# Optimization experiments

Hardware: AMD Instinct MI355X
Metric: run time of the kernel (lower is better)

The kernel has to match this reference:

```python
import jax, jax.numpy as jnp
import numpy as np

N_NODES = 100000
N_EDGES = 1600000
D_IN = 128
D_HID = 128
D_OUT = 128


def sage_conv(x, src, dst, W_l, b_l, W_r, n_nodes):
    # PyG SAGEConv (mean aggr): out = Linear_l(mean_j x_j) + Linear_r(x_i)
    msg = x[src]                                            # [E, d] gather
    agg = jax.ops.segment_sum(msg, dst, num_segments=n_nodes)  # [N, d]
    cnt = jax.ops.segment_sum(jnp.ones((src.shape[0],), x.dtype), dst,
                              num_segments=n_nodes)
    mean = agg / jnp.maximum(cnt, 1.0)[:, None]             # mean over neighbors
    return mean @ W_l.T + b_l + x @ W_r.T


def setup_inputs() -> dict:
    key = jax.random.key(0)
    ks = jax.random.split(key, 8)
    x = jax.random.normal(ks[0], (N_NODES, D_IN), dtype=jnp.float32)
    edge_index = jax.random.randint(ks[1], (2, N_EDGES), 0, N_NODES, dtype=jnp.int64)
    s1 = 1.0 / np.sqrt(D_IN)
    s2 = 1.0 / np.sqrt(D_HID)
    W1_l = jax.random.uniform(ks[2], (D_HID, D_IN), jnp.float32, -s1, s1)
    b1_l = jax.random.uniform(ks[3], (D_HID,), jnp.float32, -s1, s1)
    W1_r = jax.random.uniform(ks[4], (D_HID, D_IN), jnp.float32, -s1, s1)
    W2_l = jax.random.uniform(ks[5], (D_OUT, D_HID), jnp.float32, -s2, s2)
    b2_l = jax.random.uniform(ks[6], (D_OUT,), jnp.float32, -s2, s2)
    W2_r = jax.random.uniform(ks[7], (D_OUT, D_HID), jnp.float32, -s2, s2)
    return {"x": x, "edge_index": edge_index, "W1_l": W1_l, "b1_l": b1_l,
            "W1_r": W1_r, "W2_l": W2_l, "b2_l": b2_l, "W2_r": W2_r}


def reference(x, edge_index, W1_l, b1_l, W1_r, W2_l, b2_l, W2_r):
    src, dst = edge_index[0], edge_index[1]
    n = x.shape[0]
    h = sage_conv(x, src, dst, W1_l, b1_l, W1_r, n)
    h = jax.nn.relu(h)
    # F.dropout with training=False (eval mode) is identity
    out = sage_conv(h, src, dst, W2_l, b2_l, W2_r, n)
    return out
```

## Files before the change

### kernel.cpp

```cpp
#include <hip/hip_runtime.h>

typedef __attribute__((ext_vector_type(8))) short short8;
typedef __attribute__((ext_vector_type(4))) float f32x4;
typedef __attribute__((ext_vector_type(2))) float f32x2;

#define NBMAX 512
#define CAP 8192

__device__ inline unsigned short f2bf(float f) {
  union { float f; unsigned u; } v; v.f = f;
  unsigned r = v.u + 0x7fffu + ((v.u >> 16) & 1u);
  return (unsigned short)(r >> 16);
}

__device__ inline void addf2(f32x2 (&a)[4], uint4 v) {
  union { uint2 u; f32x2 f; } t;
  t.u.x = v.x << 16; t.u.y = v.x & 0xffff0000u; a[0] += t.f;
  t.u.x = v.y << 16; t.u.y = v.y & 0xffff0000u; a[1] += t.f;
  t.u.x = v.z << 16; t.u.y = v.z & 0xffff0000u; a[2] += t.f;
  t.u.x = v.w << 16; t.u.y = v.w & 0xffff0000u; a[3] += t.f;
}

__device__ inline int load_src(const int* ei, int E, int e, int f64) {
  return f64 ? ei[2 * e] : ei[e];
}
__device__ inline int load_dst(const int* ei, int E, int e, int f64) {
  return f64 ? ei[2 * (E + e)] : ei[E + e];
}

__global__ __launch_bounds__(256) void prep(
    const int* __restrict__ ei, int E,
    int* __restrict__ btot, int2* __restrict__ stage, int SB,
    const float* __restrict__ x, unsigned short* __restrict__ xb, int n8,
    const float* __restrict__ W1l, const float* __restrict__ W1r,
    const float* __restrict__ W2l, const float* __restrict__ W2r,
    unsigned short* __restrict__ Wp) {
  __shared__ int lcnt[NBMAX];
  __shared__ int lbase[NBMAX];
  __shared__ int sflag;
  const int b = blockIdx.x;
  const int t = threadIdx.x;

  if (b < SB) {
    if (t == 0) sflag = 0;
    for (int i = t; i < NBMAX; i += 256) lcnt[i] = 0;
    __syncthreads();
    const int e0 = b * 4096;
    {
      int e = e0 + t;
      int v = (e < E) ? ei[2 * e + 1] : 0;
      if (v) atomicOr(&sflag, 1);
    }
    __syncthreads();
    const int f64 = (sflag == 0) ? 1 : 0;

    int srcs[16], bks[16];
    int dsts[16];
#pragma unroll
    for (int i = 0; i < 16; ++i) {
      int e = e0 + i * 256 + t;
      if (e < E) {
        srcs[i] = load_src(ei, E, e, f64);
        int d = load_dst(ei, E, e, f64);
        dsts[i] = d;
        bks[i] = d >> 8;
        atomicAdd(&lcnt[d >> 8], 1);
      } else {
        bks[i] = -1;
      }
    }
    __syncthreads();
    for (int i = t; i < NBMAX; i += 256) {
      int c = lcnt[i];
      lbase[i] = c ? atomicAdd(&btot[i], c) : 0;
    }
    __syncthreads();
    for (int i = t; i < NBMAX; i += 256) lcnt[i] = 0;
    __syncthreads();
#pragma unroll
    for (int i = 0; i < 16; ++i) {
      int bk = bks[i];
      if (bk >= 0) {
        int r = atomicAdd(&lcnt[bk], 1);
        stage[(size_t)bk * CAP + lbase[bk] + r] = make_int2(srcs[i], dsts[i]);
      }
    }
    return;
  }

  if (b < SB + 4) {
    const int m = b - SB;
    const float* W = (m == 0) ? W1l : (m == 1) ? W1r : (m == 2) ? W2l : W2r;
    unsigned short* dst = Wp + (size_t)m * 16384;
#pragma unroll
    for (int it = 0; it < 8; ++it) {
      int id = it * 256 + t;
      int j = id >> 4;
      int kc = id & 15;
      int s = kc >> 2, q = kc & 3;
      int jt = j >> 4, nn2 = j & 15;
      int c = (s * 8 + jt) * 4 + q;
      const float* src = W + j * 128 + kc * 8;
      union { unsigned short u[8]; uint4 v; } tv;
#pragma unroll
      for (int k = 0; k < 8; ++k) tv.u[k] = f2bf(src[k]);
      *(uint4*)(dst + (c * 16 + nn2) * 8) = tv.v;
    }
    return;
  }

  const int cb = b - SB - 4;
  const int nxb = gridDim.x - SB - 4;
  int i = cb * 256 + t;
  const int stride = nxb * 256;
  for (; i < n8; i += stride) {
    float4 v0 = ((const float4*)x)[2 * i];
    float4 v1 = ((const float4*)x)[2 * i + 1];
    union { unsigned short u[8]; uint4 v; } tv;
    tv.u[0] = f2bf(v0.x); tv.u[1] = f2bf(v0.y);
    tv.u[2] = f2bf(v0.z); tv.u[3] = f2bf(v0.w);
    tv.u[4] = f2bf(v1.x); tv.u[5] = f2bf(v1.y);
    tv.u[6] = f2bf(v1.z); tv.u[7] = f2bf(v1.w);
    ((uint4*)xb)[i] = tv.v;
  }
}

__global__ __launch_bounds__(256) void bucket_fill2(
    const int2* __restrict__ stage, const int* __restrict__ btot,
    int* __restrict__ offs, int* __restrict__ cnt, float* __restrict__ inv,
    int* __restrict__ csr, int N) {
  __shared__ int lhist[256];
  __shared__ int lscan[256];
  __shared__ int lcur[256];
  __shared__ int red[256];
  const int b = blockIdx.x;
  const int t = threadIdx.x;
  int sum = 0;
  for (int j = t; j < b; j += 256) sum += btot[j];
  red[t] = sum;
  lhist[t] = 0;
  __syncthreads();
  for (int d = 128; d; d >>= 1) {
    if (t < d) red[t] += red[t + d];
    __syncthreads();
  }
  const int base = red[0];
  const int count = btot[b];
  const int2* sp = stage + (size_t)b * CAP;
  for (int i = t; i < count; i += 256)
    atomicAdd(&lhist[sp[i].y & 255], 1);
  __syncthreads();
  int v = lhist[t];
  lscan[t] = v;
  __syncthreads();
  for (int d = 1; d < 256; d <<= 1) {
    int tv = (t >= d) ? lscan[t - d] : 0;
    __syncthreads();
    lscan[t] += tv;
    __syncthreads();
  }
  const int excl = lscan[t] - v;
  const int node = b * 256 + t;
  if (node < N) {
    offs[node] = base + excl;
    cnt[node] = v;
    inv[node] = 1.0f / (float)((v > 1) ? v : 1);
  }
  lcur[t] = base + excl;
  __syncthreads();
  for (int i = t; i < count; i += 256) {
    int2 sd = sp[i];
    int p = atomicAdd(&lcur[sd.y & 255], 1);
    csr[p] = sd.x;
  }
}

__global__ __launch_bounds__(256, 4) void agg_mean(
    const unsigned short* __restrict__ A, const float* __restrict__ inv,
    const int* __restrict__ offs, const int* __restrict__ cnt,
    const int* __restrict__ csr, unsigned short* __restrict__ M, int n) {
  int pr = (int)((blockIdx.x * 256 + threadIdx.x) >> 6);
  int n0 = pr * 2;
  if (n0 >= n) return;
  const int n1 = n0 + 1;
  const bool has1 = (n1 < n);
  const int lane = threadIdx.x & 63;
  const int g = lane >> 4;
  const int l = lane & 15;
  const int deg0 = cnt[n0];
  const int deg1 = has1 ? cnt[n1] : 0;
  const int start = offs[n0];
  const int T = deg0 + deg1;
  f32x2 acc0[4] = {{0.f, 0.f}, {0.f, 0.f}, {0.f, 0.f}, {0.f, 0.f}};
  f32x2 acc1[4] = {{0.f, 0.f}, {0.f, 0.f}, {0.f, 0.f}, {0.f, 0.f}};
  const char* Ab = (const char*)A + (size_t)l * 16;

  if (T <= 64) {
    int offb = ((lane < T) ? csr[start + lane] : 0) << 8;
    {
      int nb[8];
      uint4 vv[8];
#pragma unroll
      for (int j = 0; j < 8; ++j) nb[j] = __shfl(offb, j * 4 + g);
#pragma unroll
      for (int j = 0; j < 8; ++j)
        vv[j] = *(const uint4*)(Ab + (size_t)(unsigned)nb[j]);
#pragma unroll
      for (int j = 0; j < 8; ++j) {
        int e = j * 4 + g;
        if (e < deg0) addf2(acc0, vv[j]);
        else if (e < T) addf2(acc1, vv[j]);
      }
    }
    if (T > 32) {
      int nb[8];
      uint4 vv[8];
#pragma unroll
      for (int j = 0; j < 8; ++j) nb[j] = __shfl(offb, 32 + j * 4 + g);
#pragma unroll
      for (int j = 0; j < 8; ++j)
        vv[j] = *(const uint4*)(Ab + (size_t)(unsigned)nb[j]);
#pragma unroll
      for (int j = 0; j < 8; ++j) {
        int e = 32 + j * 4 + g;
        if (e < deg0) addf2(acc0, vv[j]);
        else if (e < T) addf2(acc1, vv[j]);
      }
    }
  } else {
    for (int node = 0; node < 2; ++node) {
      int dg = node ? deg1 : deg0;
      int st = node ? (start + deg0) : start;
      for (int base = 0; base < dg; base += 64) {
        int m = dg - base;
        if (m > 64) m = 64;
        int offb = ((lane < m) ? csr[st + base + lane] : 0) << 8;
#pragma unroll 4
        for (int i = 0; i < m; i += 4) {
          int sl = i + g;
          int nbv = __shfl(offb, sl & 63);
          if (sl < m) {
            uint4 v = *(const uint4*)(Ab + (size_t)(unsigned)nbv);
            if (node) addf2(acc1, v);
            else addf2(acc0, v);
          }
        }
      }
    }
  }

#pragma unroll
  for (int k = 0; k < 4; ++k) {
    acc0[k].x += __shfl_xor(acc0[k].x, 16);
    acc0[k].x += __shfl_xor(acc0[k].x, 32);
    acc0[k].y += __shfl_xor(acc0[k].y, 16);
    acc0[k].y += __shfl_xor(acc0[k].y, 32);
    acc1[k].x += __shfl_xor(acc1[k].x, 16);
    acc1[k].x += __shfl_xor(acc1[k].x, 32);
    acc1[k].y += __shfl_xor(acc1[k].y, 16);
    acc1[k].y += __shfl_xor(acc1[k].y, 32);
  }

  const int c0 = l * 8 + g * 2;
  {
    float s = inv[n0];
    unsigned pkt = (unsigned)f2bf(acc0[g].x * s) |
                   ((unsigned)f2bf(acc0[g].y * s) << 16);
    *(unsigned*)(M + (size_t)n0 * 128 + c0) = pkt;
  }
  if (has1) {
    float s = inv[n1];
    unsigned pkt = (unsigned)f2bf(acc1[g].x * s) |
                   ((unsigned)f2bf(acc1[g].y * s) << 16);
    *(unsigned*)(M + (size_t)n1 * 128 + c0) = pkt;
  }
}

template <int RELU, int OUTBF>
__global__ __launch_bounds__(256) void gemm_fused(
    const unsigned short* __restrict__ Am,
    const unsigned short* __restrict__ As,
    const unsigned short* __restrict__ Wp,
    const float* __restrict__ bias, void* __restrict__ outp, int n) {
  __shared__ unsigned short wsh[2 * 16384];
  const int tid = threadIdx.x;

  {
    const uint4* wsrc = (const uint4*)Wp;
    uint4* wdst = (uint4*)wsh;
#pragma unroll
    for (int it = 0; it < 16; ++it) {
      int id = it * 256 + tid;
      wdst[id] = wsrc[id];
    }
  }
  __syncthreads();

  const int lane = tid & 63;
  const int wave = tid >> 6;
  const int nn = lane & 15;
  const int quad = lane >> 4;
  const int rowbase = blockIdx.x * 64 + wave * 16;

  int nodeA = rowbase + nn;
  if (nodeA > n - 1) nodeA = n - 1;

  short8 am[4], asf[4];
#pragma unroll
  for (int s = 0; s < 4; ++s) {
    am[s] = *(const short8*)(Am + (size_t)nodeA * 128 + s * 32 + quad * 8);
    asf[s] = *(const short8*)(As + (size_t)nodeA * 128 + s * 32 + quad * 8);
  }

  f32x4 acc[8];
#pragma unroll
  for (int jt = 0; jt < 8; ++jt) acc[jt] = (f32x4){0.f, 0.f, 0.f, 0.f};

#pragma unroll
  for (int jt = 0; jt < 8; ++jt) {
#pragma unroll
    for (int s = 0; s < 4; ++s) {
      int c = (s * 8 + jt) * 4 + quad;
      short8 bl = *(const short8*)(wsh + (c * 16 + nn) * 8);
      short8 br = *(const short8*)(wsh + 16384 + (c * 16 + nn) * 8);
      acc[jt] = __builtin_amdgcn_mfma_f32_16x16x32_bf16(am[s], bl, acc[jt], 0, 0, 0);
      acc[jt] = __builtin_amdgcn_mfma_f32_16x16x32_bf16(asf[s], br, acc[jt], 0, 0, 0);
    }
  }

#pragma unroll
  for (int jt = 0; jt < 8; ++jt) {
    int col = jt * 16 + nn;
    float bv = bias[col];
#pragma unroll
    for (int r = 0; r < 4; ++r) {
      int ro = rowbase + quad * 4 + r;
      if (ro < n) {
        float o = acc[jt][r] + bv;
        if (RELU) o = fmaxf(o, 0.f);
        if (OUTBF) {
          ((unsigned short*)outp)[(size_t)ro * 128 + col] = f2bf(o);
        } else {
          ((float*)outp)[(size_t)ro * 128 + col] = o;
        }
      }
    }
  }
}


extern "C" void kernel_launch(void* const* d_in, const int* in_sizes, int n_in,
                              void* d_out, int out_size, void* d_ws, size_t ws_size,
                              hipStream_t stream) {
  const float* x = (const float*)d_in[0];
  const int* ei = (const int*)d_in[1];
  const float* W1l = (const float*)d_in[2];
  const float* b1 = (const float*)d_in[3];
  const float* W1r = (const float*)d_in[4];
  const float* W2l = (const float*)d_in[5];
  const float* b2 = (const float*)d_in[6];
  const float* W2r = (const float*)d_in[7];
  float* out = (float*)d_out;

  const int N = in_sizes[0] / 128;
  const int E = in_sizes[1] / 2;
  const int nb = (N + 255) / 256;

  char* p = (char*)d_ws;
  auto alloc = [&](size_t bytes) {
    char* r = p;
    p += (bytes + 255) & ~(size_t)255;
    return r;
  };
  int* btot = (int*)alloc((size_t)NBMAX * 4);
  int* cnt = (int*)alloc((size_t)N * 4);
  int* offs = (int*)alloc((size_t)N * 4);
  float* inv = (float*)alloc((size_t)N * 4);
  int* csr = (int*)alloc((size_t)E * 4);
  unsigned short* Mb = (unsigned short*)alloc((size_t)N * 128 * 2);
  unsigned short* Wpb = (unsigned short*)alloc((size_t)4 * 16384 * 2);
  size_t stage_bytes = (size_t)nb * CAP * 8;
  size_t hb_bytes = (size_t)N * 128 * 2;
  char* shared_region = alloc(stage_bytes > hb_bytes ? stage_bytes : hb_bytes);
  unsigned short* hb = (unsigned short*)shared_region;
  int2* stage = (int2*)shared_region;

  unsigned short* xb = (unsigned short*)d_out;

  hipMemsetAsync(btot, 0, (size_t)nb * 4, stream);

  const int SB = (E + 4095) / 4096;
  prep<<<SB + 4 + 2048, 256, 0, stream>>>(ei, E, btot, stage, SB,
                                          x, xb, N * 128 / 8,
                                          W1l, W1r, W2l, W2r, Wpb);
  bucket_fill2<<<nb, 256, 0, stream>>>(stage, btot, offs, cnt, inv, csr, N);

  const int gb = (N + 63) / 64;
  const int pairs = (N + 1) / 2;
  const int ab2 = (pairs + 3) / 4;

  agg_mean<<<ab2, 256, 0, stream>>>(xb, inv, offs, cnt, csr, Mb, N);
  gemm_fused<1, 1><<<gb, 256, 0, stream>>>(Mb, xb, Wpb, b1, (void*)hb, N);
  agg_mean<<<ab2, 256, 0, stream>>>(hb, inv, offs, cnt, csr, Mb, N);
  gemm_fused<0, 0><<<gb, 256, 0, stream>>>(Mb, hb, Wpb + 32768, b2, (void*)out, N);
}
```

Measured before the change: 323.7 us.

## Fuse neighbor mean aggregation into the MFMA GEMM kernel per layer

Replaces the separate agg_mean and gemm_fused kernels with one agg_gemm kernel. Each lane gathers and averages the neighbor rows of its own node straight into registers as the bf16 A-operand, so the intermediate mean buffer is never written to or read back from global memory. The two weight halves are now staged one after the other through a single 32KB LDS buffer, which halves shared-memory use per block. The cost is a different gather pattern: each lane walks its node's edge list serially with only two edges in flight, and all 16 nodes in a group loop to the largest degree among them. This gives less coalescing and less memory-level parallelism than the old wavefront-per-node-pair gather.

```diff
diff --git a/kernel.cpp b/kernel.cpp
--- a/kernel.cpp
+++ b/kernel.cpp
@@ -175,126 +175,22 @@
   }
 }
 
-__global__ __launch_bounds__(256, 4) void agg_mean(
-    const unsigned short* __restrict__ A, const float* __restrict__ inv,
+template <int RELU, int OUTBF>
+__global__ __launch_bounds__(256, 4) void agg_gemm(
+    const unsigned short* __restrict__ A,
+    const unsigned short* __restrict__ Wp,
+    const float* __restrict__ bias, const float* __restrict__ inv,
     const int* __restrict__ offs, const int* __restrict__ cnt,
-    const int* __restrict__ csr, unsigned short* __restrict__ M, int n) {
-  int pr = (int)((blockIdx.x * 256 + threadIdx.x) >> 6);
-  int n0 = pr * 2;
-  if (n0 >= n) return;
-  const int n1 = n0 + 1;
-  const bool has1 = (n1 < n);
-  const int lane = threadIdx.x & 63;
-  const int g = lane >> 4;
-  const int l = lane & 15;
-  const int deg0 = cnt[n0];
-  const int deg1 = has1 ? cnt[n1] : 0;
-  const int start = offs[n0];
-  const int T = deg0 + deg1;
-  f32x2 acc0[4] = {{0.f, 0.f}, {0.f, 0.f}, {0.f, 0.f}, {0.f, 0.f}};
-  f32x2 acc1[4] = {{0.f, 0.f}, {0.f, 0.f}, {0.f, 0.f}, {0.f, 0.f}};
-  const char* Ab = (const char*)A + (size_t)l * 16;
-
-  if (T <= 64) {
-    int offb = ((lane < T) ? csr[start + lane] : 0) << 8;
-    {
-      int nb[8];
-      uint4 vv[8];
-#pragma unroll
-      for (int j = 0; j < 8; ++j) nb[j] = __shfl(offb, j * 4 + g);
-#pragma unroll
-      for (int j = 0; j < 8; ++j)
-        vv[j] = *(const uint4*)(Ab + (size_t)(unsigned)nb[j]);
-#pragma unroll
-      for (int j = 0; j < 8; ++j) {
-        int e = j * 4 + g;
-        if (e < deg0) addf2(acc0, vv[j]);
-        else if (e < T) addf2(acc1, vv[j]);
-      }
-    }
-    if (T > 32) {
-      int nb[8];
-      uint4 vv[8];
-#pragma unroll
-      for (int j = 0; j < 8; ++j) nb[j] = __shfl(offb, 32 + j * 4 + g);
-#pragma unroll
-      for (int j = 0; j < 8; ++j)
-        vv[j] = *(const uint4*)(Ab + (size_t)(unsigned)nb[j]);
-#pragma unroll
-      for (int j = 0; j < 8; ++j) {
-        int e = 32 + j * 4 + g;
-        if (e < deg0) addf2(acc0, vv[j]);
-        else if (e < T) addf2(acc1, vv[j]);
-      }
-    }
-  } else {
-    for (int node = 0; node < 2; ++node) {
-      int dg = node ? deg1 : deg0;
-      int st = node ? (start + deg0) : start;
-      for (int base = 0; base < dg; base += 64) {
-        int m = dg - base;
-        if (m > 64) m = 64;
-        int offb = ((lane < m) ? csr[st + base + lane] : 0) << 8;
-#pragma unroll 4
-        for (int i = 0; i < m; i += 4) {
-          int sl = i + g;
-          int nbv = __shfl(offb, sl & 63);
-          if (sl < m) {
-            uint4 v = *(const uint4*)(Ab + (size_t)(unsigned)nbv);
-            if (node) addf2(acc1, v);
-            else addf2(acc0, v);
-          }
-        }
-      }
-    }
-  }
-
-#pragma unroll
-  for (int k = 0; k < 4; ++k) {
-    acc0[k].x += __shfl_xor(acc0[k].x, 16);
-    acc0[k].x += __shfl_xor(acc0[k].x, 32);
-    acc0[k].y += __shfl_xor(acc0[k].y, 16);
-    acc0[k].y += __shfl_xor(acc0[k].y, 32);
-    acc1[k].x += __shfl_xor(acc1[k].x, 16);
-    acc1[k].x += __shfl_xor(acc1[k].x, 32);
-    acc1[k].y += __shfl_xor(acc1[k].y, 16);
-    acc1[k].y += __shfl_xor(acc1[k].y, 32);
-  }
-
-  const int c0 = l * 8 + g * 2;
-  {
-    float s = inv[n0];
-    unsigned pkt = (unsigned)f2bf(acc0[g].x * s) |
-                   ((unsigned)f2bf(acc0[g].y * s) << 16);
-    *(unsigned*)(M + (size_t)n0 * 128 + c0) = pkt;
-  }
-  if (has1) {
-    float s = inv[n1];
-    unsigned pkt = (unsigned)f2bf(acc1[g].x * s) |
-                   ((unsigned)f2bf(acc1[g].y * s) << 16);
-    *(unsigned*)(M + (size_t)n1 * 128 + c0) = pkt;
-  }
-}
-
-template <int RELU, int OUTBF>
-__global__ __launch_bounds__(256) void gemm_fused(
-    const unsigned short* __restrict__ Am,
-    const unsigned short* __restrict__ As,
-    const unsigned short* __restrict__ Wp,
-    const float* __restrict__ bias, void* __restrict__ outp, int n) {
-  __shared__ unsigned short wsh[2 * 16384];
+    const int* __restrict__ csr, void* __restrict__ outp, int n) {
+  __shared__ unsigned short wsh[16384];
   const int tid = threadIdx.x;
 
   {
     const uint4* wsrc = (const uint4*)Wp;
     uint4* wdst = (uint4*)wsh;
 #pragma unroll
-    for (int it = 0; it < 16; ++it) {
-      int id = it * 256 + tid;
-      wdst[id] = wsrc[id];
-    }
-  }
-  __syncthreads();
+    for (int it = 0; it < 8; ++it) wdst[it * 256 + tid] = wsrc[it * 256 + tid];
+  }
 
   const int lane = tid & 63;
   const int wave = tid >> 6;
@@ -305,16 +201,70 @@
   int nodeA = rowbase + nn;
   if (nodeA > n - 1) nodeA = n - 1;
 
-  short8 am[4], asf[4];
+  short8 asf[4];
+#pragma unroll
+  for (int s = 0; s < 4; ++s)
+    asf[s] = *(const short8*)(A + (size_t)nodeA * 128 + s * 32 + quad * 8);
+
+  const int deg = cnt[nodeA];
+  const int off0 = offs[nodeA];
+  const float sc = inv[nodeA];
+
+  int md = deg;
+  md = max(md, __shfl_xor(md, 1));
+  md = max(md, __shfl_xor(md, 2));
+  md = max(md, __shfl_xor(md, 4));
+  md = max(md, __shfl_xor(md, 8));
+
+  f32x2 acc[4][4];
+#pragma unroll
+  for (int s = 0; s < 4; ++s)
+#pragma unroll
+    for (int p = 0; p < 4; ++p) acc[s][p] = (f32x2){0.f, 0.f};
+
+  const char* Abase = (const char*)A;
+  const int qoff = quad * 16;
+
+  int i0 = (0 < deg) ? csr[off0] : 0;
+  int i1 = (1 < deg) ? csr[off0 + 1] : 0;
+  for (int j = 0; j < md; j += 2) {
+    int ni0 = (j + 2 < deg) ? csr[off0 + j + 2] : 0;
+    int ni1 = (j + 3 < deg) ? csr[off0 + j + 3] : 0;
+    const char* p0 = Abase + ((size_t)(unsigned)i0 << 8) + qoff;
+    const char* p1 = Abase + ((size_t)(unsigned)i1 << 8) + qoff;
+    uint4 v0[4], v1[4];
+#pragma unroll
+    for (int s = 0; s < 4; ++s) v0[s] = *(const uint4*)(p0 + s * 64);
+#pragma unroll
+    for (int s = 0; s < 4; ++s) v1[s] = *(const uint4*)(p1 + s * 64);
+    if (j < deg) {
+#pragma unroll
+      for (int s = 0; s < 4; ++s) addf2(acc[s], v0[s]);
+    }
+    if (j + 1 < deg) {
+#pragma unroll
+      for (int s = 0; s < 4; ++s) addf2(acc[s], v1[s]);
+    }
+    i0 = ni0; i1 = ni1;
+  }
+
+  short8 am[4];
 #pragma unroll
   for (int s = 0; s < 4; ++s) {
-    am[s] = *(const short8*)(Am + (size_t)nodeA * 128 + s * 32 + quad * 8);
-    asf[s] = *(const short8*)(As + (size_t)nodeA * 128 + s * 32 + quad * 8);
-  }
-
-  f32x4 acc[8];
-#pragma unroll
-  for (int jt = 0; jt < 8; ++jt) acc[jt] = (f32x4){0.f, 0.f, 0.f, 0.f};
+    union { unsigned short u[8]; short8 v; } t;
+#pragma unroll
+    for (int p = 0; p < 4; ++p) {
+      t.u[2 * p] = f2bf(acc[s][p].x * sc);
+      t.u[2 * p + 1] = f2bf(acc[s][p].y * sc);
+    }
+    am[s] = t.v;
+  }
+
+  f32x4 accc[8];
+#pragma unroll
+  for (int jt = 0; jt < 8; ++jt) accc[jt] = (f32x4){0.f, 0.f, 0.f, 0.f};
+
+  __syncthreads();
 
 #pragma unroll
   for (int jt = 0; jt < 8; ++jt) {
@@ -322,9 +272,27 @@
     for (int s = 0; s < 4; ++s) {
       int c = (s * 8 + jt) * 4 + quad;
       short8 bl = *(const short8*)(wsh + (c * 16 + nn) * 8);
-      short8 br = *(const short8*)(wsh + 16384 + (c * 16 + nn) * 8);
-      acc[jt] = __builtin_amdgcn_mfma_f32_16x16x32_bf16(am[s], bl, acc[jt], 0, 0, 0);
-      acc[jt] = __builtin_amdgcn_mfma_f32_16x16x32_bf16(asf[s], br, acc[jt], 0, 0, 0);
+      accc[jt] = __builtin_amdgcn_mfma_f32_16x16x32_bf16(am[s], bl, accc[jt], 0, 0, 0);
+    }
+  }
+
+  __syncthreads();
+
+  {
+    const uint4* wsrc = (const uint4*)(Wp + 16384);
+    uint4* wdst = (uint4*)wsh;
+#pragma unroll
+    for (int it = 0; it < 8; ++it) wdst[it * 256 + tid] = wsrc[it * 256 + tid];
+  }
+  __syncthreads();
+
+#pragma unroll
+  for (int jt = 0; jt < 8; ++jt) {
+#pragma unroll
+    for (int s = 0; s < 4; ++s) {
+      int c = (s * 8 + jt) * 4 + quad;
+      short8 br = *(const short8*)(wsh + (c * 16 + nn) * 8);
+      accc[jt] = __builtin_amdgcn_mfma_f32_16x16x32_bf16(asf[s], br, accc[jt], 0, 0, 0);
     }
   }
 
@@ -336,7 +304,7 @@
     for (int r = 0; r < 4; ++r) {
       int ro = rowbase + quad * 4 + r;
       if (ro < n) {
-        float o = acc[jt][r] + bv;
+        float o = accc[jt][r] + bv;
         if (RELU) o = fmaxf(o, 0.f);
         if (OUTBF) {
           ((unsigned short*)outp)[(size_t)ro * 128 + col] = f2bf(o);
@@ -377,7 +345,6 @@
   int* offs = (int*)alloc((size_t)N * 4);
   float* inv = (float*)alloc((size_t)N * 4);
   int* csr = (int*)alloc((size_t)E * 4);
-  unsigned short* Mb = (unsigned short*)alloc((size_t)N * 128 * 2);
   unsigned short* Wpb = (unsigned short*)alloc((size_t)4 * 16384 * 2);
   size_t stage_bytes = (size_t)nb * CAP * 8;
   size_t hb_bytes = (size_t)N * 128 * 2;
@@ -396,11 +363,9 @@
   bucket_fill2<<<nb, 256, 0, stream>>>(stage, btot, offs, cnt, inv, csr, N);
 
   const int gb = (N + 63) / 64;
-  const int pairs = (N + 1) / 2;
-  const int ab2 = (pairs + 3) / 4;
-
-  agg_mean<<<ab2, 256, 0, stream>>>(xb, inv, offs, cnt, csr, Mb, N);
-  gemm_fused<1, 1><<<gb, 256, 0, stream>>>(Mb, xb, Wpb, b1, (void*)hb, N);
-  agg_mean<<<ab2, 256, 0, stream>>>(hb, inv, offs, cnt, csr, Mb, N);
-  gemm_fused<0, 0><<<gb, 256, 0, stream>>>(Mb, hb, Wpb + 32768, b2, (void*)out, N);
-}
+
+  agg_gemm<1, 1><<<gb, 256, 0, stream>>>(xb, Wpb, b1, inv, offs, cnt, csr,
+                                         (void*)hb, N);
+  agg_gemm<0, 0><<<gb, 256, 0, stream>>>(hb, Wpb + 32768, b2, inv, offs, cnt, csr,
+                                         (void*)out, N);
+}
```

Measured after the change: 329.4 us. About the same (+1.8%).

## Fuse all stages into one cooperative persistent kernel with grid syncs

Applied to the files above, without the earlier changes.

Replaces the six separate launches (prep, bucket fill, two aggregations, two GEMMs) with a single cooperative kernel of 512-thread blocks that loops over work units and separates stages with grid-wide barriers. The aim is to remove kernel launch gaps and per-kernel ramp-up and tail costs. In exchange, each block reserves 64KB of shared memory and the grid is capped to resident blocks, which can lower occupancy for the latency-bound gather phases, and every grid barrier drains the whole device.

```diff
diff --git a/kernel.cpp b/kernel.cpp
--- a/kernel.cpp
+++ b/kernel.cpp
@@ -1,4 +1,7 @@
 #include <hip/hip_runtime.h>
+#include <hip/hip_cooperative_groups.h>
+
+namespace cg = cooperative_groups;
 
 typedef __attribute__((ext_vector_type(8))) short short8;
 typedef __attribute__((ext_vector_type(4))) float f32x4;
@@ -28,92 +31,252 @@
   return f64 ? ei[2 * (E + e)] : ei[E + e];
 }
 
-__global__ __launch_bounds__(256) void prep(
-    const int* __restrict__ ei, int E,
-    int* __restrict__ btot, int2* __restrict__ stage, int SB,
-    const float* __restrict__ x, unsigned short* __restrict__ xb, int n8,
-    const float* __restrict__ W1l, const float* __restrict__ W1r,
-    const float* __restrict__ W2l, const float* __restrict__ W2r,
-    unsigned short* __restrict__ Wp) {
-  __shared__ int lcnt[NBMAX];
-  __shared__ int lbase[NBMAX];
-  __shared__ int sflag;
-  const int b = blockIdx.x;
+__device__ void agg_phase(const unsigned short* __restrict__ A,
+                          const float* __restrict__ inv,
+                          const int* __restrict__ offs,
+                          const int* __restrict__ cnt,
+                          const int* __restrict__ csr,
+                          unsigned short* __restrict__ M, int n) {
   const int t = threadIdx.x;
-
-  if (b < SB) {
-    if (t == 0) sflag = 0;
-    for (int i = t; i < NBMAX; i += 256) lcnt[i] = 0;
-    __syncthreads();
-    const int e0 = b * 4096;
+  const int lane = t & 63;
+  const int wave = t >> 6;
+  const int g = lane >> 4;
+  const int l = lane & 15;
+  const char* Ab = (const char*)A + (size_t)l * 16;
+  const int units = (((n + 1) >> 1) + 7) >> 3;
+
+  for (int u = blockIdx.x; u < units; u += gridDim.x) {
+    const int pr = u * 8 + wave;
+    const int n0 = pr * 2;
+    if (n0 >= n) continue;
+    const int n1 = n0 + 1;
+    const bool has1 = (n1 < n);
+    const int deg0 = cnt[n0];
+    const int deg1 = has1 ? cnt[n1] : 0;
+    const int start = offs[n0];
+    const int T = deg0 + deg1;
+    f32x2 acc0[4] = {{0.f, 0.f}, {0.f, 0.f}, {0.f, 0.f}, {0.f, 0.f}};
+    f32x2 acc1[4] = {{0.f, 0.f}, {0.f, 0.f}, {0.f, 0.f}, {0.f, 0.f}};
+
+    if (T <= 64) {
+      int offb = ((lane < T) ? csr[start + lane] : 0) << 8;
+      {
+        int nb2[8];
+        uint4 vv[8];
+#pragma unroll
+        for (int j = 0; j < 8; ++j) nb2[j] = __shfl(offb, j * 4 + g);
+#pragma unroll
+        for (int j = 0; j < 8; ++j)
+          vv[j] = *(const uint4*)(Ab + (size_t)(unsigned)nb2[j]);
+#pragma unroll
+        for (int j = 0; j < 8; ++j) {
+          int e = j * 4 + g;
+          if (e < deg0) addf2(acc0, vv[j]);
+          else if (e < T) addf2(acc1, vv[j]);
+        }
+      }
+      if (T > 32) {
+        int nb2[8];
+        uint4 vv[8];
+#pragma unroll
+        for (int j = 0; j < 8; ++j) nb2[j] = __shfl(offb, 32 + j * 4 + g);
+#pragma unroll
+        for (int j = 0; j < 8; ++j)
+          vv[j] = *(const uint4*)(Ab + (size_t)(unsigned)nb2[j]);
+#pragma unroll
+        for (int j = 0; j < 8; ++j) {
+          int e = 32 + j * 4 + g;
+          if (e < deg0) addf2(acc0, vv[j]);
+          else if (e < T) addf2(acc1, vv[j]);
+        }
+      }
+    } else {
+      for (int node = 0; node < 2; ++node) {
+        int dg = node ? deg1 : deg0;
+        int st = node ? (start + deg0) : start;
+        for (int base = 0; base < dg; base += 64) {
+          int m = dg - base;
+          if (m > 64) m = 64;
+          int offb = ((lane < m) ? csr[st + base + lane] : 0) << 8;
+#pragma unroll 4
+          for (int i = 0; i < m; i += 4) {
+            int sl = i + g;
+            int nbv = __shfl(offb, sl & 63);
+            if (sl < m) {
+              uint4 v = *(const uint4*)(Ab + (size_t)(unsigned)nbv);
+              if (node) addf2(acc1, v);
+              else addf2(acc0, v);
+            }
+          }
+        }
+      }
+    }
+
+#pragma unroll
+    for (int k = 0; k < 4; ++k) {
+      acc0[k].x += __shfl_xor(acc0[k].x, 16);
+      acc0[k].x += __shfl_xor(acc0[k].x, 32);
+      acc0[k].y += __shfl_xor(acc0[k].y, 16);
+      acc0[k].y += __shfl_xor(acc0[k].y, 32);
+      acc1[k].x += __shfl_xor(acc1[k].x, 16);
+      acc1[k].x += __shfl_xor(acc1[k].x, 32);
+      acc1[k].y += __shfl_xor(acc1[k].y, 16);
+      acc1[k].y += __shfl_xor(acc1[k].y, 32);
+    }
+
+    const int c0 = l * 8 + g * 2;
     {
-      int e = e0 + t;
-      int v = (e < E) ? ei[2 * e + 1] : 0;
-      if (v) atomicOr(&sflag, 1);
-    }
-    __syncthreads();
-    const int f64 = (sflag == 0) ? 1 : 0;
-
-    int srcs[16], bks[16];
-    int dsts[16];
-#pragma unroll
-    for (int i = 0; i < 16; ++i) {
-      int e = e0 + i * 256 + t;
-      if (e < E) {
-        srcs[i] = load_src(ei, E, e, f64);
-        int d = load_dst(ei, E, e, f64);
-        dsts[i] = d;
-        bks[i] = d >> 8;
-        atomicAdd(&lcnt[d >> 8], 1);
-      } else {
-        bks[i] = -1;
-      }
-    }
-    __syncthreads();
-    for (int i = t; i < NBMAX; i += 256) {
-      int c = lcnt[i];
-      lbase[i] = c ? atomicAdd(&btot[i], c) : 0;
-    }
-    __syncthreads();
-    for (int i = t; i < NBMAX; i += 256) lcnt[i] = 0;
-    __syncthreads();
-#pragma unroll
-    for (int i = 0; i < 16; ++i) {
-      int bk = bks[i];
-      if (bk >= 0) {
-        int r = atomicAdd(&lcnt[bk], 1);
-        stage[(size_t)bk * CAP + lbase[bk] + r] = make_int2(srcs[i], dsts[i]);
-      }
-    }
-    return;
-  }
-
-  if (b < SB + 4) {
-    const int m = b - SB;
-    const float* W = (m == 0) ? W1l : (m == 1) ? W1r : (m == 2) ? W2l : W2r;
-    unsigned short* dst = Wp + (size_t)m * 16384;
-#pragma unroll
-    for (int it = 0; it < 8; ++it) {
-      int id = it * 256 + t;
-      int j = id >> 4;
-      int kc = id & 15;
-      int s = kc >> 2, q = kc & 3;
-      int jt = j >> 4, nn2 = j & 15;
-      int c = (s * 8 + jt) * 4 + q;
-      const float* src = W + j * 128 + kc * 8;
-      union { unsigned short u[8]; uint4 v; } tv;
-#pragma unroll
-      for (int k = 0; k < 8; ++k) tv.u[k] = f2bf(src[k]);
-      *(uint4*)(dst + (c * 16 + nn2) * 8) = tv.v;
-    }
-    return;
-  }
-
-  const int cb = b - SB - 4;
-  const int nxb = gridDim.x - SB - 4;
-  int i = cb * 256 + t;
-  const int stride = nxb * 256;
-  for (; i < n8; i += stride) {
+      float s = inv[n0];
+      unsigned pkt = (unsigned)f2bf(acc0[g].x * s) |
+                     ((unsigned)f2bf(acc0[g].y * s) << 16);
+      *(unsigned*)(M + (size_t)n0 * 128 + c0) = pkt;
+    }
+    if (has1) {
+      float s = inv[n1];
+      unsigned pkt = (unsigned)f2bf(acc1[g].x * s) |
+                     ((unsigned)f2bf(acc1[g].y * s) << 16);
+      *(unsigned*)(M + (size_t)n1 * 128 + c0) = pkt;
+    }
+  }
+}
+
+template <int RELU, int OUTBF>
+__device__ void gemm_phase(const unsigned short* __restrict__ Am,
+                           const unsigned short* __restrict__ As,
+                           const unsigned short* __restrict__ Wp,
+                           const float* __restrict__ bias,
+                           void* __restrict__ outp, int n,
+                           unsigned short* wsh) {
+  const int tid = threadIdx.x;
+  {
+    const uint4* wsrc = (const uint4*)Wp;
+    uint4* wdst = (uint4*)wsh;
+#pragma unroll
+    for (int it = 0; it < 8; ++it)
+      wdst[it * 512 + tid] = wsrc[it * 512 + tid];
+  }
+  __syncthreads();
+
+  const int lane = tid & 63;
+  const int wave = tid >> 6;
+  const int nn = lane & 15;
+  const int quad = lane >> 4;
+  const int nch = (n + 127) >> 7;
+
+  for (int ch = blockIdx.x; ch < nch; ch += gridDim.x) {
+    const int rowbase = ch * 128 + wave * 16;
+    int nodeA = rowbase + nn;
+    if (nodeA > n - 1) nodeA = n - 1;
+
+    short8 am[4], asf[4];
+#pragma unroll
+    for (int s = 0; s < 4; ++s) {
+      am[s] = *(const short8*)(Am + (size_t)nodeA * 128 + s * 32 + quad * 8);
+      asf[s] = *(const short8*)(As + (size_t)nodeA * 128 + s * 32 + quad * 8);
+    }
+
+    f32x4 acc[8];
+#pragma unroll
+    for (int jt = 0; jt < 8; ++jt) acc[jt] = (f32x4){0.f, 0.f, 0.f, 0.f};
+
+#pragma unroll
+    for (int jt = 0; jt < 8; ++jt) {
+#pragma unroll
+      for (int s = 0; s < 4; ++s) {
+        int c = (s * 8 + jt) * 4 + quad;
+        short8 bl = *(const short8*)(wsh + (c * 16 + nn) * 8);
+        short8 br = *(const short8*)(wsh + 16384 + (c * 16 + nn) * 8);
+        acc[jt] = __builtin_amdgcn_mfma_f32_16x16x32_bf16(am[s], bl, acc[jt], 0, 0, 0);
+        acc[jt] = __builtin_amdgcn_mfma_f32_16x16x32_bf16(asf[s], br, acc[jt], 0, 0, 0);
+      }
+    }
+
+#pragma unroll
+    for (int jt = 0; jt < 8; ++jt) {
+      int col = jt * 16 + nn;
+      float bv = bias[col];
+#pragma unroll
+      for (int r = 0; r < 4; ++r) {
+        int ro = rowbase + quad * 4 + r;
+        if (ro < n) {
+          float o = acc[jt][r] + bv;
+          if (RELU) o = fmaxf(o, 0.f);
+          if (OUTBF) {
+            ((unsigned short*)outp)[(size_t)ro * 128 + col] = f2bf(o);
+          } else {
+            ((float*)outp)[(size_t)ro * 128 + col] = o;
+          }
+        }
+      }
+    }
+  }
+}
+
+__global__ __launch_bounds__(512, 4) void mega(
+    const int* __restrict__ ei, int E, int SB, int N, int nb, int n8,
+    const float* __restrict__ x,
+    const float* __restrict__ W1l, const float* __restrict__ b1,
+    const float* __restrict__ W1r, const float* __restrict__ W2l,
+    const float* __restrict__ b2, const float* __restrict__ W2r,
+    int* btot, int2* stage, int* cnt, int* offs, float* inv, int* csr,
+    unsigned short* Mb, unsigned short* Wp, unsigned short* xb,
+    unsigned short* hb, float* out) {
+  __shared__ __align__(16) int sbuf[16384];
+  cg::grid_group gg = cg::this_grid();
+  const int t = threadIdx.x;
+
+  {
+    int* lcnt = sbuf;
+    int* lbase = sbuf + NBMAX;
+    int* sflag = sbuf + 2 * NBMAX;
+    for (int c = blockIdx.x; c < SB; c += gridDim.x) {
+      if (t == 0) *sflag = 0;
+      for (int i = t; i < NBMAX; i += 512) lcnt[i] = 0;
+      __syncthreads();
+      const int e0 = c * 4096;
+      {
+        int e = e0 + t;
+        int v = (e < E) ? ei[2 * e + 1] : 0;
+        if (v) atomicOr(sflag, 1);
+      }
+      __syncthreads();
+      const int f64 = (*sflag == 0) ? 1 : 0;
+
+      int srcs[8], bks[8], dsts[8];
+#pragma unroll
+      for (int i = 0; i < 8; ++i) {
+        int e = e0 + i * 512 + t;
+        if (e < E) {
+          srcs[i] = load_src(ei, E, e, f64);
+          int d = load_dst(ei, E, e, f64);
+          dsts[i] = d;
+          bks[i] = d >> 8;
+          atomicAdd(&lcnt[d >> 8], 1);
+        } else {
+          bks[i] = -1;
+        }
+      }
+      __syncthreads();
+      for (int i = t; i < NBMAX; i += 512) {
+        int cc = lcnt[i];
+        lbase[i] = cc ? atomicAdd(&btot[i], cc) : 0;
+      }
+      __syncthreads();
+      for (int i = t; i < NBMAX; i += 512) lcnt[i] = 0;
+      __syncthreads();
+#pragma unroll
+      for (int i = 0; i < 8; ++i) {
+        int bk = bks[i];
+        if (bk >= 0) {
+          int r = atomicAdd(&lcnt[bk], 1);
+          stage[(size_t)bk * CAP + lbase[bk] + r] = make_int2(srcs[i], dsts[i]);
+        }
+      }
+      __syncthreads();
+    }
+  }
+
+  for (int i = blockIdx.x * 512 + t; i < n8; i += gridDim.x * 512) {
     float4 v0 = ((const float4*)x)[2 * i];
     float4 v1 = ((const float4*)x)[2 * i + 1];
     union { unsigned short u[8]; uint4 v; } tv;
@@ -123,229 +286,96 @@
     tv.u[6] = f2bf(v1.z); tv.u[7] = f2bf(v1.w);
     ((uint4*)xb)[i] = tv.v;
   }
-}
-
-__global__ __launch_bounds__(256) void bucket_fill2(
-    const int2* __restrict__ stage, const int* __restrict__ btot,
-    int* __restrict__ offs, int* __restrict__ cnt, float* __restrict__ inv,
-    int* __restrict__ csr, int N) {
-  __shared__ int lhist[256];
-  __shared__ int lscan[256];
-  __shared__ int lcur[256];
-  __shared__ int red[256];
-  const int b = blockIdx.x;
-  const int t = threadIdx.x;
-  int sum = 0;
-  for (int j = t; j < b; j += 256) sum += btot[j];
-  red[t] = sum;
-  lhist[t] = 0;
-  __syncthreads();
-  for (int d = 128; d; d >>= 1) {
-    if (t < d) red[t] += red[t + d];
-    __syncthreads();
-  }
-  const int base = red[0];
-  const int count = btot[b];
-  const int2* sp = stage + (size_t)b * CAP;
-  for (int i = t; i < count; i += 256)
-    atomicAdd(&lhist[sp[i].y & 255], 1);
-  __syncthreads();
-  int v = lhist[t];
-  lscan[t] = v;
-  __syncthreads();
-  for (int d = 1; d < 256; d <<= 1) {
-    int tv = (t >= d) ? lscan[t - d] : 0;
-    __syncthreads();
-    lscan[t] += tv;
-    __syncthreads();
-  }
-  const int excl = lscan[t] - v;
-  const int node = b * 256 + t;
-  if (node < N) {
-    offs[node] = base + excl;
-    cnt[node] = v;
-    inv[node] = 1.0f / (float)((v > 1) ? v : 1);
-  }
-  lcur[t] = base + excl;
-  __syncthreads();
-  for (int i = t; i < count; i += 256) {
-    int2 sd = sp[i];
-    int p = atomicAdd(&lcur[sd.y & 255], 1);
-    csr[p] = sd.x;
-  }
-}
-
-__global__ __launch_bounds__(256, 4) void agg_mean(
-    const unsigned short* __restrict__ A, const float* __restrict__ inv,
-    const int* __restrict__ offs, const int* __restrict__ cnt,
-    const int* __restrict__ csr, unsigned short* __restrict__ M, int n) {
-  int pr = (int)((blockIdx.x * 256 + threadIdx.x) >> 6);
-  int n0 = pr * 2;
-  if (n0 >= n) return;
-  const int n1 = n0 + 1;
-  const bool has1 = (n1 < n);
-  const int lane = threadIdx.x & 63;
-  const int g = lane >> 4;
-  const int l = lane & 15;
-  const int deg0 = cnt[n0];
-  const int deg1 = has1 ? cnt[n1] : 0;
-  const int start = offs[n0];
-  const int T = deg0 + deg1;
-  f32x2 acc0[4] = {{0.f, 0.f}, {0.f, 0.f}, {0.f, 0.f}, {0.f, 0.f}};
-  f32x2 acc1[4] = {{0.f, 0.f}, {0.f, 0.f}, {0.f, 0.f}, {0.f, 0.f}};
-  const char* Ab = (const char*)A + (size_t)l * 16;
-
-  if (T <= 64) {
-    int offb = ((lane < T) ? csr[start + lane] : 0) << 8;
-    {
-      int nb[8];
-      uint4 vv[8];
-#pragma unroll
-      for (int j = 0; j < 8; ++j) nb[j] = __shfl(offb, j * 4 + g);
-#pragma unroll
-      for (int j = 0; j < 8; ++j)
-        vv[j] = *(const uint4*)(Ab + (size_t)(unsigned)nb[j]);
-#pragma unroll
-      for (int j = 0; j < 8; ++j) {
-        int e = j * 4 + g;
-        if (e < deg0) addf2(acc0, vv[j]);
-        else if (e < T) addf2(acc1, vv[j]);
-      }
-    }
-    if (T > 32) {
-      int nb[8];
-      uint4 vv[8];
-#pragma unroll
-      for (int j = 0; j < 8; ++j) nb[j] = __shfl(offb, 32 + j * 4 + g);
-#pragma unroll
-      for (int j = 0; j < 8; ++j)
-        vv[j] = *(const uint4*)(Ab + (size_t)(unsigned)nb[j]);
-#pragma unroll
-      for (int j = 0; j < 8; ++j) {
-        int e = 32 + j * 4 + g;
-        if (e < deg0) addf2(acc0, vv[j]);
-        else if (e < T) addf2(acc1, vv[j]);
-      }
-    }
-  } else {
-    for (int node = 0; node < 2; ++node) {
-      int dg = node ? deg1 : deg0;
-      int st = node ? (start + deg0) : start;
-      for (int base = 0; base < dg; base += 64) {
-        int m = dg - base;
-        if (m > 64) m = 64;
-        int offb = ((lane < m) ? csr[st + base + lane] : 0) << 8;
-#pragma unroll 4
-        for (int i = 0; i < m; i += 4) {
-          int sl = i + g;
-          int nbv = __shfl(offb, sl & 63);
-          if (sl < m) {
-            uint4 v = *(const uint4*)(Ab + (size_t)(unsigned)nbv);
-            if (node) addf2(acc1, v);
-            else addf2(acc0, v);
-          }
-        }
-      }
-    }
-  }
-
-#pragma unroll
-  for (int k = 0; k < 4; ++k) {
-    acc0[k].x += __shfl_xor(acc0[k].x, 16);
-    acc0[k].x += __shfl_xor(acc0[k].x, 32);
-    acc0[k].y += __shfl_xor(acc0[k].y, 16);
-    acc0[k].y += __shfl_xor(acc0[k].y, 32);
-    acc1[k].x += __shfl_xor(acc1[k].x, 16);
-    acc1[k].x += __shfl_xor(acc1[k].x, 32);
-    acc1[k].y += __shfl_xor(acc1[k].y, 16);
-    acc1[k].y += __shfl_xor(acc1[k].y, 32);
-  }
-
-  const int c0 = l * 8 + g * 2;
+
+  if (blockIdx.x < 4) {
+    const int m = blockIdx.x;
+    const float* W = (m == 0) ? W1l : (m == 1) ? W1r : (m == 2) ? W2l : W2r;
+    unsigned short* dst = Wp + (size_t)m * 16384;
+#pragma unroll
+    for (int it = 0; it < 4; ++it) {
+      int id = it * 512 + t;
+      int j = id >> 4;
+      int kc = id & 15;
+      int s = kc >> 2, q = kc & 3;
+      int jt = j >> 4, nn2 = j & 15;
+      int c = (s * 8 + jt) * 4 + q;
+      const float* src = W + j * 128 + kc * 8;
+      union { unsigned short u[8]; uint4 v; } tv;
+#pragma unroll
+      for (int k = 0; k < 8; ++k) tv.u[k] = f2bf(src[k]);
+      *(uint4*)(dst + (c * 16 + nn2) * 8) = tv.v;
+    }
+  }
+
+  __threadfence();
+  gg.sync();
+
   {
-    float s = inv[n0];
-    unsigned pkt = (unsigned)f2bf(acc0[g].x * s) |
-                   ((unsigned)f2bf(acc0[g].y * s) << 16);
-    *(unsigned*)(M + (size_t)n0 * 128 + c0) = pkt;
-  }
-  if (has1) {
-    float s = inv[n1];
-    unsigned pkt = (unsigned)f2bf(acc1[g].x * s) |
-                   ((unsigned)f2bf(acc1[g].y * s) << 16);
-    *(unsigned*)(M + (size_t)n1 * 128 + c0) = pkt;
-  }
-}
-
-template <int RELU, int OUTBF>
-__global__ __launch_bounds__(256) void gemm_fused(
-    const unsigned short* __restrict__ Am,
-    const unsigned short* __restrict__ As,
-    const unsigned short* __restrict__ Wp,
-    const float* __restrict__ bias, void* __restrict__ outp, int n) {
-  __shared__ unsigned short wsh[2 * 16384];
-  const int tid = threadIdx.x;
-
-  {
-    const uint4* wsrc = (const uint4*)Wp;
-    uint4* wdst = (uint4*)wsh;
-#pragma unroll
-    for (int it = 0; it < 16; ++it) {
-      int id = it * 256 + tid;
-      wdst[id] = wsrc[id];
-    }
-  }
-  __syncthreads();
-
-  const int lane = tid & 63;
-  const int wave = tid >> 6;
-  const int nn = lane & 15;
-  const int quad = lane >> 4;
-  const int rowbase = blockIdx.x * 64 + wave * 16;
-
-  int nodeA = rowbase + nn;
-  if (nodeA > n - 1) nodeA = n - 1;
-
-  short8 am[4], asf[4];
-#pragma unroll
-  for (int s = 0; s < 4; ++s) {
-    am[s] = *(const short8*)(Am + (size_t)nodeA * 128 + s * 32 + quad * 8);
-    asf[s] = *(const short8*)(As + (size_t)nodeA * 128 + s * 32 + quad * 8);
-  }
-
-  f32x4 acc[8];
-#pragma unroll
-  for (int jt = 0; jt < 8; ++jt) acc[jt] = (f32x4){0.f, 0.f, 0.f, 0.f};
-
-#pragma unroll
-  for (int jt = 0; jt < 8; ++jt) {
-#pragma unroll
-    for (int s = 0; s < 4; ++s) {
-      int c = (s * 8 + jt) * 4 + quad;
-      short8 bl = *(const short8*)(wsh + (c * 16 + nn) * 8);
-      short8 br = *(const short8*)(wsh + 16384 + (c * 16 + nn) * 8);
-      acc[jt] = __builtin_amdgcn_mfma_f32_16x16x32_bf16(am[s], bl, acc[jt], 0, 0, 0);
-      acc[jt] = __builtin_amdgcn_mfma_f32_16x16x32_bf16(asf[s], br, acc[jt], 0, 0, 0);
-    }
-  }
-
-#pragma unroll
-  for (int jt = 0; jt < 8; ++jt) {
-    int col = jt * 16 + nn;
-    float bv = bias[col];
-#pragma unroll
-    for (int r = 0; r < 4; ++r) {
-      int ro = rowbase + quad * 4 + r;
-      if (ro < n) {
-        float o = acc[jt][r] + bv;
-        if (RELU) o = fmaxf(o, 0.f);
-        if (OUTBF) {
-          ((unsigned short*)outp)[(size_t)ro * 128 + col] = f2bf(o);
-        } else {
-          ((float*)outp)[(size_t)ro * 128 + col] = o;
-        }
-      }
-    }
-  }
+    int* lhist = sbuf;
+    int* lscan = sbuf + 256;
+    int* lcur = sbuf + 512;
+    int* red = sbuf + 768;
+    for (int b = blockIdx.x; b < nb; b += gridDim.x) {
+      int sum = 0;
+      for (int j = t; j < b; j += 512) sum += btot[j];
+      red[t] = sum;
+      if (t < 256) lhist[t] = 0;
+      __syncthreads();
+      for (int d = 256; d; d >>= 1) {
+        if (t < d) red[t] += red[t + d];
+        __syncthreads();
+      }
+      const int base = red[0];
+      const int count = btot[b];
+      const int2* sp = stage + (size_t)b * CAP;
+      for (int i = t; i < count; i += 512)
+        atomicAdd(&lhist[sp[i].y & 255], 1);
+      __syncthreads();
+      int v = (t < 256) ? lhist[t] : 0;
+      if (t < 256) lscan[t] = v;
+      __syncthreads();
+      for (int d = 1; d < 256; d <<= 1) {
+        int tv = (t >= d && t < 256) ? lscan[t - d] : 0;
+        __syncthreads();
+        if (t < 256) lscan[t] += tv;
+        __syncthreads();
+      }
+      if (t < 256) {
+        const int excl = lscan[t] - v;
+        const int node = b * 256 + t;
+        if (node < N) {
+          offs[node] = base + excl;
+          cnt[node] = v;
+          inv[node] = 1.0f / (float)((v > 1) ? v : 1);
+        }
+        lcur[t] = base + excl;
+      }
+      __syncthreads();
+      for (int i = t; i < count; i += 512) {
+        int2 sd = sp[i];
+        int p2 = atomicAdd(&lcur[sd.y & 255], 1);
+        csr[p2] = sd.x;
+      }
+      __syncthreads();
+    }
+  }
+
+  __threadfence();
+  gg.sync();
+
+  agg_phase(xb, inv, offs, cnt, csr, Mb, N);
+  __threadfence();
+  gg.sync();
+
+  gemm_phase<1, 1>(Mb, xb, Wp, b1, (void*)hb, N, (unsigned short*)sbuf);
+  __threadfence();
+  gg.sync();
+
+  agg_phase(hb, inv, offs, cnt, csr, Mb, N);
+  __threadfence();
+  gg.sync();
+
+  gemm_phase<0, 0>(Mb, hb, Wp + 32768, b2, (void*)out, N, (unsigned short*)sbuf);
 }
 
 
@@ -384,23 +414,35 @@
   char* shared_region = alloc(stage_bytes > hb_bytes ? stage_bytes : hb_bytes);
   unsigned short* hb = (unsigned short*)shared_region;
   int2* stage = (int2*)shared_region;
-
   unsigned short* xb = (unsigned short*)d_out;
 
+  const int SB = (E + 4095) / 4096;
+  const int n8 = N * 128 / 8;
+
+  static int coop_grid = 0;
+  if (coop_grid == 0) {
+    int dev = 0;
+    hipGetDevice(&dev);
+    hipDeviceProp_t props;
+    hipGetDeviceProperties(&props, dev);
+    int bpm = 0;
+    if (hipOccupancyMaxActiveBlocksPerMultiprocessor(&bpm, mega, 512, 0) != hipSuccess || bpm <= 0)
+      bpm = 1;
+    long g = (long)bpm * props.multiProcessorCount;
+    if (g < 64) g = 64;
+    if (g > 2048) g = 2048;
+    coop_grid = (int)g;
+  }
+
   hipMemsetAsync(btot, 0, (size_t)nb * 4, stream);
 
-  const int SB = (E + 4095) / 4096;
-  prep<<<SB + 4 + 2048, 256, 0, stream>>>(ei, E, btot, stage, SB,
-                                          x, xb, N * 128 / 8,
-                                          W1l, W1r, W2l, W2r, Wpb);
-  bucket_fill2<<<nb, 256, 0, stream>>>(stage, btot, offs, cnt, inv, csr, N);
-
-  const int gb = (N + 63) / 64;
-  const int pairs = (N + 1) / 2;
-  const int ab2 = (pairs + 3) / 4;
-
-  agg_mean<<<ab2, 256, 0, stream>>>(xb, inv, offs, cnt, csr, Mb, N);
-  gemm_fused<1, 1><<<gb, 256, 0, stream>>>(Mb, xb, Wpb, b1, (void*)hb, N);
-  agg_mean<<<ab2, 256, 0, stream>>>(hb, inv, offs, cnt, csr, Mb, N);
-  gemm_fused<0, 0><<<gb, 256, 0, stream>>>(Mb, hb, Wpb + 32768, b2, (void*)out, N);
-}
+  int E_ = E, SB_ = SB, N_ = N, nb_ = nb, n8_ = n8;
+  void* args[] = {
+      (void*)&ei, (void*)&E_, (void*)&SB_, (void*)&N_, (void*)&nb_, (void*)&n8_,
+      (void*)&x, (void*)&W1l, (void*)&b1, (void*)&W1r, (void*)&W2l,
+      (void*)&b2, (void*)&W2r, (void*)&btot, (void*)&stage, (void*)&cnt,
+      (void*)&offs, (void*)&inv, (void*)&csr, (void*)&Mb, (void*)&Wpb,
+      (void*)&xb, (void*)&hb, (void*)&out};
+  hipLaunchCooperativeKernel((const void*)mega, dim3(coop_grid), dim3(512),
+                             args, 0, stream);
+}
```

After: 1.047 ms. +223.5%, slower.

## Pack staged edges into 32-bit words, halve edges per block, overlap gathers

Applied to the files above, without the earlier changes.

Staged edge records go from an int2 (src, dst) to one 32-bit word holding the source shifted left by 8 and the low 8 bits of the destination. This halves the staging buffer's write and read traffic between prep and bucket_fill2. Each prep block now handles 2048 edges instead of 4096, doubling the number of scatter blocks. In agg_mean, both 32-neighbor gather batches are issued before any accumulation so more loads are in flight, at the cost of more registers. The packing relies on node ids fitting in 24 bits.

```diff
diff --git a/kernel.cpp b/kernel.cpp
--- a/kernel.cpp
+++ b/kernel.cpp
@@ -30,7 +30,7 @@
 
 __global__ __launch_bounds__(256) void prep(
     const int* __restrict__ ei, int E,
-    int* __restrict__ btot, int2* __restrict__ stage, int SB,
+    int* __restrict__ btot, unsigned* __restrict__ stage, int SB,
     const float* __restrict__ x, unsigned short* __restrict__ xb, int n8,
     const float* __restrict__ W1l, const float* __restrict__ W1r,
     const float* __restrict__ W2l, const float* __restrict__ W2r,
@@ -45,7 +45,7 @@
     if (t == 0) sflag = 0;
     for (int i = t; i < NBMAX; i += 256) lcnt[i] = 0;
     __syncthreads();
-    const int e0 = b * 4096;
+    const int e0 = b * 2048;
     {
       int e = e0 + t;
       int v = (e < E) ? ei[2 * e + 1] : 0;
@@ -54,15 +54,15 @@
     __syncthreads();
     const int f64 = (sflag == 0) ? 1 : 0;
 
-    int srcs[16], bks[16];
-    int dsts[16];
-#pragma unroll
-    for (int i = 0; i < 16; ++i) {
+    unsigned pk[8];
+    int bks[8];
+#pragma unroll
+    for (int i = 0; i < 8; ++i) {
       int e = e0 + i * 256 + t;
       if (e < E) {
-        srcs[i] = load_src(ei, E, e, f64);
+        int s = load_src(ei, E, e, f64);
         int d = load_dst(ei, E, e, f64);
-        dsts[i] = d;
+        pk[i] = ((unsigned)s << 8) | ((unsigned)d & 255u);
         bks[i] = d >> 8;
         atomicAdd(&lcnt[d >> 8], 1);
       } else {
@@ -78,11 +78,11 @@
     for (int i = t; i < NBMAX; i += 256) lcnt[i] = 0;
     __syncthreads();
 #pragma unroll
-    for (int i = 0; i < 16; ++i) {
+    for (int i = 0; i < 8; ++i) {
       int bk = bks[i];
       if (bk >= 0) {
         int r = atomicAdd(&lcnt[bk], 1);
-        stage[(size_t)bk * CAP + lbase[bk] + r] = make_int2(srcs[i], dsts[i]);
+        stage[(size_t)bk * CAP + lbase[bk] + r] = pk[i];
       }
     }
     return;
@@ -126,7 +126,7 @@
 }
 
 __global__ __launch_bounds__(256) void bucket_fill2(
-    const int2* __restrict__ stage, const int* __restrict__ btot,
+    const unsigned* __restrict__ stage, const int* __restrict__ btot,
     int* __restrict__ offs, int* __restrict__ cnt, float* __restrict__ inv,
     int* __restrict__ csr, int N) {
   __shared__ int lhist[256];
@@ -146,9 +146,9 @@
   }
   const int base = red[0];
   const int count = btot[b];
-  const int2* sp = stage + (size_t)b * CAP;
+  const unsigned* sp = stage + (size_t)b * CAP;
   for (int i = t; i < count; i += 256)
-    atomicAdd(&lhist[sp[i].y & 255], 1);
+    atomicAdd(&lhist[sp[i] & 255u], 1);
   __syncthreads();
   int v = lhist[t];
   lscan[t] = v;
@@ -169,9 +169,9 @@
   lcur[t] = base + excl;
   __syncthreads();
   for (int i = t; i < count; i += 256) {
-    int2 sd = sp[i];
-    int p = atomicAdd(&lcur[sd.y & 255], 1);
-    csr[p] = sd.x;
+    unsigned sd = sp[i];
+    int p = atomicAdd(&lcur[sd & 255u], 1);
+    csr[p] = (int)(sd >> 8);
   }
 }
 
@@ -197,34 +197,35 @@
 
   if (T <= 64) {
     int offb = ((lane < T) ? csr[start + lane] : 0) << 8;
-    {
-      int nb[8];
-      uint4 vv[8];
-#pragma unroll
-      for (int j = 0; j < 8; ++j) nb[j] = __shfl(offb, j * 4 + g);
+    const bool twoB = (T > 32);
+    int nbA[8], nbB[8];
+    uint4 vA[8], vB[8];
+#pragma unroll
+    for (int j = 0; j < 8; ++j) nbA[j] = __shfl(offb, j * 4 + g);
+    if (twoB) {
+#pragma unroll
+      for (int j = 0; j < 8; ++j) nbB[j] = __shfl(offb, 32 + j * 4 + g);
+    }
+#pragma unroll
+    for (int j = 0; j < 8; ++j)
+      vA[j] = *(const uint4*)(Ab + (size_t)(unsigned)nbA[j]);
+    if (twoB) {
 #pragma unroll
       for (int j = 0; j < 8; ++j)
-        vv[j] = *(const uint4*)(Ab + (size_t)(unsigned)nb[j]);
-#pragma unroll
-      for (int j = 0; j < 8; ++j) {
-        int e = j * 4 + g;
-        if (e < deg0) addf2(acc0, vv[j]);
-        else if (e < T) addf2(acc1, vv[j]);
-      }
-    }
-    if (T > 32) {
-      int nb[8];
-      uint4 vv[8];
-#pragma unroll
-      for (int j = 0; j < 8; ++j) nb[j] = __shfl(offb, 32 + j * 4 + g);
-#pragma unroll
-      for (int j = 0; j < 8; ++j)
-        vv[j] = *(const uint4*)(Ab + (size_t)(unsigned)nb[j]);
+        vB[j] = *(const uint4*)(Ab + (size_t)(unsigned)nbB[j]);
+    }
+#pragma unroll
+    for (int j = 0; j < 8; ++j) {
+      int e = j * 4 + g;
+      if (e < deg0) addf2(acc0, vA[j]);
+      else if (e < T) addf2(acc1, vA[j]);
+    }
+    if (twoB) {
 #pragma unroll
       for (int j = 0; j < 8; ++j) {
         int e = 32 + j * 4 + g;
-        if (e < deg0) addf2(acc0, vv[j]);
-        else if (e < T) addf2(acc1, vv[j]);
+        if (e < deg0) addf2(acc0, vB[j]);
+        else if (e < T) addf2(acc1, vB[j]);
       }
     }
   } else {
@@ -379,17 +380,17 @@
   int* csr = (int*)alloc((size_t)E * 4);
   unsigned short* Mb = (unsigned short*)alloc((size_t)N * 128 * 2);
   unsigned short* Wpb = (unsigned short*)alloc((size_t)4 * 16384 * 2);
-  size_t stage_bytes = (size_t)nb * CAP * 8;
+  size_t stage_bytes = (size_t)nb * CAP * 4;
   size_t hb_bytes = (size_t)N * 128 * 2;
   char* shared_region = alloc(stage_bytes > hb_bytes ? stage_bytes : hb_bytes);
   unsigned short* hb = (unsigned short*)shared_region;
-  int2* stage = (int2*)shared_region;
+  unsigned* stage = (unsigned*)shared_region;
 
   unsigned short* xb = (unsigned short*)d_out;
 
   hipMemsetAsync(btot, 0, (size_t)nb * 4, stream);
 
-  const int SB = (E + 4095) / 4096;
+  const int SB = (E + 2047) / 2048;
   prep<<<SB + 4 + 2048, 256, 0, stream>>>(ei, E, btot, stage, SB,
                                           x, xb, N * 128 / 8,
                                           W1l, W1r, W2l, W2r, Wpb);
```

Measured after the change: 343.1 us. 1.06x slower.
